# Kernel tuning notes

Measured on AMD Instinct MI355X. Metric: run time of the kernel, lower is better.

## Reference

```python
import jax, jax.numpy as jnp
import numpy as np
import math

B, S, E = 16, 4096, 16      # batch, seq_len, n_experts
NE = 64                     # config.n_embd -> expert bottleneck dim
F = 4 * NE                  # n_state = 4*n_embd -> token feature dim


def gelu(x):
    # tanh-approx GELU exactly as in the source module
    c = math.sqrt(2.0 / math.pi)
    return 0.5 * x * (1.0 + jnp.tanh(c * (x + 0.044715 * x * x * x)))


def setup_inputs() -> dict:
    key = jax.random.key(0)
    ks = jax.random.split(key, 7)
    s1 = 1.0 / math.sqrt(F)   # fan-in init like nn.Linear(F, NE)
    s2 = 1.0 / math.sqrt(NE)  # fan-in init like nn.Linear(NE, F)
    return {
        "x":  jax.random.normal(ks[0], (B, S, F), jnp.float32),
        "W1": jax.random.uniform(ks[1], (E, F, NE), jnp.float32, -s1, s1),  # stacked c_fc
        "b1": jax.random.uniform(ks[2], (E, NE),    jnp.float32, -s1, s1),
        "W2": jax.random.uniform(ks[3], (E, NE, F), jnp.float32, -s2, s2),  # stacked c_proj
        "b2": jax.random.uniform(ks[4], (E, F),     jnp.float32, -s2, s2),
        "Wg": jax.random.uniform(ks[5], (F, E),     jnp.float32, -s1, s1),  # router
        "bg": jax.random.uniform(ks[6], (E,),       jnp.float32, -s1, s1),
    }


def reference(x, W1, b1, W2, b2, Wg, bg):
    # Router: per-token scores -> mean over sequence -> softmax over experts. [B, E]
    gate = jax.nn.softmax(jnp.mean(x @ Wg + bg, axis=1), axis=-1)
    # Dense all-experts FFN: [B, E, S, NE]
    h = gelu(jnp.einsum('bsf,efh->besh', x, W1) + b1[None, :, None, :])
    # [B, E, S, F]
    outs = jnp.einsum('besh,ehf->besf', h, W2) + b2[None, :, None, :]
    # Gate-weighted combine over experts -> [B, S, F]
    return jnp.einsum('be,besf->bsf', gate, outs)
```

## Files before the change

kernel.cpp:

```cpp
#include <hip/hip_runtime.h>
#include <hip/hip_bf16.h>
#include <stdint.h>

#define NB 16
#define NS 4096
#define NF 256
#define NH 64
#define NEXP 16

typedef __attribute__((ext_vector_type(8))) short     bf16x8;
typedef __attribute__((ext_vector_type(4))) float     f32x4;
typedef __attribute__((ext_vector_type(2))) unsigned  u32x2;
typedef __attribute__((ext_vector_type(8))) unsigned short u16x8;

#define PART_OFF   0u
#define GATE_OFF   524288u
#define BIASC_OFF  525312u
#define W1T_OFF    541696u
#define W2T_OFF    1065984u

__device__ __forceinline__ unsigned short bfr(float f) {
  unsigned u = __float_as_uint(f);
  u += 0x7fffu + ((u >> 16) & 1u);
  return (unsigned short)(u >> 16);
}
__device__ __forceinline__ unsigned pk(float a, float b) {
  __hip_bfloat162 t = __float22bfloat162_rn(make_float2(a, b));
  union { __hip_bfloat162 h; unsigned u; } cv; cv.h = t; return cv.u;
}
__device__ __forceinline__ bf16x8 as_bf(f32x4 v) {
  union { f32x4 f; bf16x8 h; } u; u.f = v; return u.h;
}
__device__ __forceinline__ void stage16(const void* g, void* l) {
  __builtin_amdgcn_global_load_lds((const __attribute__((address_space(1))) void*)g,
                                   (__attribute__((address_space(3))) void*)l, 16, 0, 0);
}

__global__ void k_pre(const float* __restrict__ x, const float* __restrict__ W1,
                      const float* __restrict__ W2, uint8_t* __restrict__ wsb) {
  const int blk = blockIdx.x;
  if (blk < 512) {
    const int b  = blk >> 5;
    const int ch = blk & 31;
    const int f  = threadIdx.x;
    const float* xp = x + ((size_t)b * NS + (size_t)ch * 128) * NF + f;
    float s = 0.0f;
    for (int i = 0; i < 128; ++i) s += xp[(size_t)i * NF];
    ((float*)(wsb + PART_OFF))[(size_t)(ch * 16 + b) * NF + f] = s;
    return;
  }
  const int u = (blk - 512) * 256 + threadIdx.x;
  u16x8 vals;
  if (u < 32768) {
    const int e  = u >> 11;
    const int r  = u & 2047;
    const int hd = r >> 5;
    const int kc = r & 31;
    const float* src = W1 + (size_t)e * (NF * NH) + (size_t)(kc * 8) * NH + hd;
#pragma unroll
    for (int j = 0; j < 8; ++j) vals[j] = bfr(src[(size_t)j * NH]);
    const int dst = (kc >> 2) * 4096 + hd * 64 + (kc & 3) * 16;
    *(u16x8*)(wsb + W1T_OFF + (size_t)e * 32768 + dst) = vals;
  } else {
    const int u2 = u - 32768;
    const int e  = u2 >> 11;
    const int r  = u2 & 2047;
    const int f  = r >> 3;
    const int hc = r & 7;
    const float* src = W2 + (size_t)e * (NH * NF) + (size_t)(hc * 8) * NF + f;
#pragma unroll
    for (int j = 0; j < 8; ++j) vals[j] = bfr(src[(size_t)j * NF]);
    const int dst = hc * 4096 + f * 16;
    *(u16x8*)(wsb + W2T_OFF + (size_t)e * 32768 + dst) = vals;
  }
}

__global__ void k_gate(const float* __restrict__ Wg, const float* __restrict__ bg,
                       const float* __restrict__ b2, uint8_t* __restrict__ wsb) {
  __shared__ float cs[16][256];
  __shared__ float lg[16][16];
  __shared__ float gs[16][16];
  const float* part  = (const float*)(wsb + PART_OFF);
  float* gate  = (float*)(wsb + GATE_OFF);
  float* biasc = (float*)(wsb + BIASC_OFF);
  const int t = threadIdx.x;
  for (int b = 0; b < 16; ++b) {
    float s = 0.0f;
    for (int ch = 0; ch < 32; ++ch) s += part[(size_t)(ch * 16 + b) * NF + t];
    cs[b][t] = s * (1.0f / 4096.0f);
  }
  __syncthreads();
  {
    const int b = t >> 4, e = t & 15;
    float acc = bg[e];
    for (int f = 0; f < NF; ++f) acc += cs[b][f] * Wg[f * 16 + e];
    lg[b][e] = acc;
  }
  __syncthreads();
  {
    const int b = t >> 4, e = t & 15;
    float m = lg[b][0];
    for (int j = 1; j < 16; ++j) m = fmaxf(m, lg[b][j]);
    float den = 0.0f;
    for (int j = 0; j < 16; ++j) den += __expf(lg[b][j] - m);
    float g = __expf(lg[b][e] - m) / den;
    gate[b * 16 + e] = g;
    gs[b][e] = g;
  }
  __syncthreads();
  for (int b = 0; b < 16; ++b) {
    float acc = 0.0f;
    for (int e = 0; e < 16; ++e) acc += gs[b][e] * b2[e * NF + t];
    biasc[b * NF + t] = acc;
  }
}

__global__ __launch_bounds__(512, 2)
void k_main(const float* __restrict__ x, const float* __restrict__ b1g,
            const uint8_t* __restrict__ wsb, float* __restrict__ out) {
  __shared__ __align__(16) uint8_t lds[98304];

  const int tid  = threadIdx.x;
  const int w    = tid >> 6;
  const int lane = tid & 63;
  const int c    = lane & 15;
  const int q    = lane >> 4;
  const int r4   = w & 3;
  const bool g1  = (w < 4);
  const int blk  = blockIdx.x;
  const int b    = blk >> 5;

  const float* gate_ws = (const float*)(wsb + GATE_OFF) + b * 16;
  const float* biasc   = (const float*)(wsb + BIASC_OFF) + b * NF;
  const uint8_t* w1src = wsb + W1T_OFF;
  const uint8_t* w2src = wsb + W2T_OFF;

  const f32x4 fz = {0.0f, 0.0f, 0.0f, 0.0f};
  f32x4 R[32];

#pragma unroll
  for (int i = 0; i < 4; ++i)
    stage16(w1src + i * 8192 + tid * 16, lds + i * 8192 + tid * 16);

  if (g1) {
    const int row0 = blk * 128 + r4 * 32;
#pragma unroll
    for (int n = 0; n < 2; ++n) {
      const float* xp = x + (size_t)(row0 + n * 16 + c) * NF + q * 8;
#pragma unroll
      for (int ks = 0; ks < 8; ++ks) {
        f32x4 v0 = *(const f32x4*)(xp + ks * 32);
        f32x4 v1 = *(const f32x4*)(xp + ks * 32 + 4);
        union { unsigned u[4]; f32x4 f; } cv;
        cv.u[0] = pk(v0[0], v0[1]); cv.u[1] = pk(v0[2], v0[3]);
        cv.u[2] = pk(v1[0], v1[1]); cv.u[3] = pk(v1[2], v1[3]);
        R[8 + n * 8 + ks] = cv.f;
      }
    }
  } else {
#pragma unroll
    for (int i = 0; i < 32; ++i) R[i] = fz;
  }

  bf16x8 w2r[2][4];

  __syncthreads();

  const float K1 = -2.3021858962f;
  const float KA = -0.102942243f;

#pragma unroll 1
  for (int e = 0; e < NEXP; ++e) {
    const int p  = e & 1;
    const int pn = p ^ 1;

    if (e < 15) {
      const uint8_t* src = w1src + (size_t)(e + 1) * 32768;
      uint8_t* dst = lds + pn * 32768;
#pragma unroll
      for (int i = 0; i < 4; ++i)
        stage16(src + i * 8192 + tid * 16, dst + i * 8192 + tid * 16);
    }

    if (g1) {
      const uint8_t* w1p = lds + p * 32768;
#pragma unroll
      for (int i = 0; i < 8; ++i) R[i] = fz;
      __builtin_amdgcn_s_setprio(1);
#pragma unroll
      for (int ks = 0; ks < 8; ++ks) {
        bf16x8 am[4];
#pragma unroll
        for (int m = 0; m < 4; ++m)
          am[m] = *(const bf16x8*)(w1p + ks * 4096 + (m * 16 + c) * 64 + q * 16);
#pragma unroll
        for (int m = 0; m < 4; ++m) {
          R[m * 2 + 0] = __builtin_amdgcn_mfma_f32_16x16x32_bf16(am[m], as_bf(R[8 + ks]),     R[m * 2 + 0], 0, 0, 0);
          R[m * 2 + 1] = __builtin_amdgcn_mfma_f32_16x16x32_bf16(am[m], as_bf(R[16 + ks]),    R[m * 2 + 1], 0, 0, 0);
        }
      }
      __builtin_amdgcn_s_setprio(0);

      const float gv = gate_ws[e];
      uint8_t* htp = lds + 65536 + p * 16384;
#pragma unroll
      for (int m = 0; m < 4; ++m) {
        f32x4 b1v = *(const f32x4*)(b1g + e * NH + m * 16 + q * 4);
#pragma unroll
        for (int n = 0; n < 2; ++n) {
          f32x4 hv = R[m * 2 + n] + b1v;
          float o[4];
#pragma unroll
          for (int r = 0; r < 4; ++r) {
            float xx = hv[r];
            float x2 = xx * xx;
            float tt = fmaf(KA, x2, K1);
            float ez = __builtin_amdgcn_exp2f(xx * tt);
            float rc = __builtin_amdgcn_rcpf(ez + 1.0f);
            o[r] = (gv * xx) * rc;
          }
          u32x2 hw;
          hw.x = pk(o[0], o[1]);
          hw.y = pk(o[2], o[3]);
          const int chunk = m * 2 + (q >> 1);
          const int tok   = r4 * 32 + n * 16 + c;
          *(u32x2*)(htp + chunk * 2048 + tok * 16 + (q & 1) * 8) = hw;
        }
      }
    } else {
      if (e > 0) {
        const uint8_t* htp2 = lds + 65536 + pn * 16384;
        __builtin_amdgcn_s_setprio(1);
#pragma unroll
        for (int ks2 = 0; ks2 < 2; ++ks2) {
          bf16x8 bb2[8];
#pragma unroll
          for (int n2 = 0; n2 < 8; ++n2)
            bb2[n2] = *(const bf16x8*)(htp2 + (ks2 * 4 + q) * 2048 + (n2 * 16 + c) * 16);
#pragma unroll
          for (int m2 = 0; m2 < 4; ++m2)
#pragma unroll
            for (int n2 = 0; n2 < 8; ++n2)
              R[m2 * 8 + n2] = __builtin_amdgcn_mfma_f32_16x16x32_bf16(w2r[ks2][m2], bb2[n2], R[m2 * 8 + n2], 0, 0, 0);
        }
        __builtin_amdgcn_s_setprio(0);
      }
      const uint8_t* src = w2src + (size_t)e * 32768 + q * 4096 + (r4 * 64 + c) * 16;
#pragma unroll
      for (int ks2 = 0; ks2 < 2; ++ks2)
#pragma unroll
        for (int m2 = 0; m2 < 4; ++m2)
          w2r[ks2][m2] = *(const bf16x8*)(src + ks2 * 16384 + m2 * 256);
    }

    __syncthreads();
  }

  if (!g1) {
    const uint8_t* htp2 = lds + 65536 + 16384;
#pragma unroll
    for (int ks2 = 0; ks2 < 2; ++ks2) {
      bf16x8 bb2[8];
#pragma unroll
      for (int n2 = 0; n2 < 8; ++n2)
        bb2[n2] = *(const bf16x8*)(htp2 + (ks2 * 4 + q) * 2048 + (n2 * 16 + c) * 16);
#pragma unroll
      for (int m2 = 0; m2 < 4; ++m2)
#pragma unroll
        for (int n2 = 0; n2 < 8; ++n2)
          R[m2 * 8 + n2] = __builtin_amdgcn_mfma_f32_16x16x32_bf16(w2r[ks2][m2], bb2[n2], R[m2 * 8 + n2], 0, 0, 0);
    }
#pragma unroll
    for (int m2 = 0; m2 < 4; ++m2) {
      const int fbase = r4 * 64 + m2 * 16 + q * 4;
      f32x4 bc = *(const f32x4*)(biasc + fbase);
#pragma unroll
      for (int n2 = 0; n2 < 8; ++n2) {
        const int token = blk * 128 + n2 * 16 + c;
        f32x4 o = R[m2 * 8 + n2] + bc;
        *(f32x4*)(out + (size_t)token * NF + fbase) = o;
      }
    }
  }
}

extern "C" void kernel_launch(void* const* d_in, const int* in_sizes, int n_in,
                              void* d_out, int out_size, void* d_ws, size_t ws_size,
                              hipStream_t stream) {
  const float* x  = (const float*)d_in[0];
  const float* W1 = (const float*)d_in[1];
  const float* b1 = (const float*)d_in[2];
  const float* W2 = (const float*)d_in[3];
  const float* b2 = (const float*)d_in[4];
  const float* Wg = (const float*)d_in[5];
  const float* bg = (const float*)d_in[6];
  float* out = (float*)d_out;
  uint8_t* wsb = (uint8_t*)d_ws;

  k_pre<<<768, 256, 0, stream>>>(x, W1, W2, wsb);
  k_gate<<<1, 256, 0, stream>>>(Wg, bg, b2, wsb);
  k_main<<<512, 512, 0, stream>>>(x, b1, wsb, out);
}
```

Measured before the change: 126.7 us.

## Skew GELU epilogue one expert behind GEMM1 with triple-buffered hidden tiles

Restructures the expert loop so the first warp group runs expert e's GEMM1 while writing the GELU epilogue for expert e-1. The hidden buffer grows from double to triple (more LDS), and the second warp group consumes hidden tiles two experts behind. The loop is unrolled by two so register slots are fixed at compile time, and W2 fragments are held in the shared R array. The goal is to overlap transcendental epilogue work with MFMA work and lengthen the pipeline, at the cost of more LDS, which may limit occupancy at two blocks per CU, and more register pressure.

Result: slower. 130.4 us (+3.0%).

```diff
diff --git a/kernel.cpp b/kernel.cpp
--- a/kernel.cpp
+++ b/kernel.cpp
@@ -115,18 +115,105 @@
   }
 }
 
+
+template<int PAR>
+__device__ __forceinline__ void g1_gemm(int e, f32x4 (&R)[40], float (&gvv)[2],
+                                        const uint8_t* ldsb, const float* b1g,
+                                        const float* gate_ws, int c, int q) {
+#pragma unroll
+  for (int m = 0; m < 4; ++m)
+    R[32 + PAR * 4 + m] = *(const f32x4*)(b1g + e * NH + m * 16 + q * 4);
+  gvv[PAR] = gate_ws[e];
+  const uint8_t* w1p = ldsb + PAR * 32768;
+  const f32x4 fz = {0.0f, 0.0f, 0.0f, 0.0f};
+#pragma unroll
+  for (int i = 0; i < 8; ++i) R[16 + PAR * 8 + i] = fz;
+  __builtin_amdgcn_s_setprio(1);
+#pragma unroll
+  for (int ks = 0; ks < 8; ++ks) {
+    bf16x8 am[4];
+#pragma unroll
+    for (int m = 0; m < 4; ++m)
+      am[m] = *(const bf16x8*)(w1p + ks * 4096 + (m * 16 + c) * 64 + q * 16);
+#pragma unroll
+    for (int m = 0; m < 4; ++m) {
+      R[16 + PAR * 8 + m * 2 + 0] = __builtin_amdgcn_mfma_f32_16x16x32_bf16(am[m], as_bf(R[ks]),     R[16 + PAR * 8 + m * 2 + 0], 0, 0, 0);
+      R[16 + PAR * 8 + m * 2 + 1] = __builtin_amdgcn_mfma_f32_16x16x32_bf16(am[m], as_bf(R[8 + ks]), R[16 + PAR * 8 + m * 2 + 1], 0, 0, 0);
+    }
+  }
+  __builtin_amdgcn_s_setprio(0);
+}
+
+template<int PPREV>
+__device__ __forceinline__ void g1_epilogue(int eprev, f32x4 (&R)[40], const float (&gvv)[2],
+                                            uint8_t* ldsb, int w, int c, int q) {
+  const float K1 = -2.3021858962f;
+  const float KA = -0.102942243f;
+  const float gv = gvv[PPREV];
+  uint8_t* htp = ldsb + 65536 + (eprev % 3) * 16384;
+#pragma unroll
+  for (int m = 0; m < 4; ++m) {
+    f32x4 b1v = R[32 + PPREV * 4 + m];
+#pragma unroll
+    for (int n = 0; n < 2; ++n) {
+      f32x4 hv = R[16 + PPREV * 8 + m * 2 + n] + b1v;
+      float o[4];
+#pragma unroll
+      for (int r = 0; r < 4; ++r) {
+        float xx = hv[r];
+        float tt = fmaf(KA, xx * xx, K1);
+        float ez = __builtin_amdgcn_exp2f(xx * tt);
+        o[r] = (gv * xx) * __builtin_amdgcn_rcpf(ez + 1.0f);
+      }
+      u32x2 hw;
+      hw.x = pk(o[0], o[1]);
+      hw.y = pk(o[2], o[3]);
+      const int chunk = m * 2 + (q >> 1);
+      const int tok   = w * 32 + n * 16 + c;
+      *(u32x2*)(htp + chunk * 2048 + tok * 16 + (q & 1) * 8) = hw;
+    }
+  }
+}
+
+__device__ __forceinline__ void g2_gemm2(f32x4 (&R)[40], const uint8_t* htp2, int c, int q) {
+#pragma unroll
+  for (int ks2 = 0; ks2 < 2; ++ks2) {
+    bf16x8 bb[8];
+#pragma unroll
+    for (int n2 = 0; n2 < 8; ++n2)
+      bb[n2] = *(const bf16x8*)(htp2 + (ks2 * 4 + q) * 2048 + (n2 * 16 + c) * 16);
+    __builtin_amdgcn_s_setprio(1);
+#pragma unroll
+    for (int m2 = 0; m2 < 4; ++m2)
+#pragma unroll
+      for (int n2 = 0; n2 < 8; ++n2)
+        R[m2 * 8 + n2] = __builtin_amdgcn_mfma_f32_16x16x32_bf16(as_bf(R[32 + ks2 * 4 + m2]), bb[n2], R[m2 * 8 + n2], 0, 0, 0);
+    __builtin_amdgcn_s_setprio(0);
+  }
+}
+
+__device__ __forceinline__ void g2_loadw2(f32x4 (&R)[40], const uint8_t* w2src, int e,
+                                          int fs, int c, int q) {
+  const uint8_t* src = w2src + (size_t)e * 32768 + q * 4096 + (fs + c) * 16;
+#pragma unroll
+  for (int ks2 = 0; ks2 < 2; ++ks2)
+#pragma unroll
+    for (int m2 = 0; m2 < 4; ++m2)
+      R[32 + ks2 * 4 + m2] = *(const f32x4*)(src + ks2 * 16384 + m2 * 256);
+}
+
 __global__ __launch_bounds__(512, 2)
 void k_main(const float* __restrict__ x, const float* __restrict__ b1g,
             const uint8_t* __restrict__ wsb, float* __restrict__ out) {
-  __shared__ __align__(16) uint8_t lds[98304];
+  __shared__ __align__(16) uint8_t lds[114688];
 
   const int tid  = threadIdx.x;
   const int w    = tid >> 6;
   const int lane = tid & 63;
   const int c    = lane & 15;
   const int q    = lane >> 4;
-  const int r4   = w & 3;
   const bool g1  = (w < 4);
+  const int fs   = (w - 4) * 64;
   const int blk  = blockIdx.x;
   const int b    = blk >> 5;
 
@@ -135,15 +222,15 @@
   const uint8_t* w1src = wsb + W1T_OFF;
   const uint8_t* w2src = wsb + W2T_OFF;
 
-  const f32x4 fz = {0.0f, 0.0f, 0.0f, 0.0f};
-  f32x4 R[32];
+  f32x4 R[40];
+  float gvv[2];
 
 #pragma unroll
   for (int i = 0; i < 4; ++i)
     stage16(w1src + i * 8192 + tid * 16, lds + i * 8192 + tid * 16);
 
   if (g1) {
-    const int row0 = blk * 128 + r4 * 32;
+    const int row0 = blk * 128 + w * 32;
 #pragma unroll
     for (int n = 0; n < 2; ++n) {
       const float* xp = x + (size_t)(row0 + n * 16 + c) * NF + q * 8;
@@ -154,125 +241,69 @@
         union { unsigned u[4]; f32x4 f; } cv;
         cv.u[0] = pk(v0[0], v0[1]); cv.u[1] = pk(v0[2], v0[3]);
         cv.u[2] = pk(v1[0], v1[1]); cv.u[3] = pk(v1[2], v1[3]);
-        R[8 + n * 8 + ks] = cv.f;
+        R[n * 8 + ks] = cv.f;
       }
     }
   } else {
+    const f32x4 fz = {0.0f, 0.0f, 0.0f, 0.0f};
 #pragma unroll
     for (int i = 0; i < 32; ++i) R[i] = fz;
   }
 
-  bf16x8 w2r[2][4];
-
-  __syncthreads();
-
-  const float K1 = -2.3021858962f;
-  const float KA = -0.102942243f;
+  __syncthreads();
 
 #pragma unroll 1
-  for (int e = 0; e < NEXP; ++e) {
-    const int p  = e & 1;
-    const int pn = p ^ 1;
-
-    if (e < 15) {
-      const uint8_t* src = w1src + (size_t)(e + 1) * 32768;
-      uint8_t* dst = lds + pn * 32768;
-#pragma unroll
-      for (int i = 0; i < 4; ++i)
-        stage16(src + i * 8192 + tid * 16, dst + i * 8192 + tid * 16);
-    }
-
-    if (g1) {
-      const uint8_t* w1p = lds + p * 32768;
-#pragma unroll
-      for (int i = 0; i < 8; ++i) R[i] = fz;
-      __builtin_amdgcn_s_setprio(1);
-#pragma unroll
-      for (int ks = 0; ks < 8; ++ks) {
-        bf16x8 am[4];
-#pragma unroll
-        for (int m = 0; m < 4; ++m)
-          am[m] = *(const bf16x8*)(w1p + ks * 4096 + (m * 16 + c) * 64 + q * 16);
-#pragma unroll
-        for (int m = 0; m < 4; ++m) {
-          R[m * 2 + 0] = __builtin_amdgcn_mfma_f32_16x16x32_bf16(am[m], as_bf(R[8 + ks]),     R[m * 2 + 0], 0, 0, 0);
-          R[m * 2 + 1] = __builtin_amdgcn_mfma_f32_16x16x32_bf16(am[m], as_bf(R[16 + ks]),    R[m * 2 + 1], 0, 0, 0);
-        }
-      }
-      __builtin_amdgcn_s_setprio(0);
-
-      const float gv = gate_ws[e];
-      uint8_t* htp = lds + 65536 + p * 16384;
-#pragma unroll
-      for (int m = 0; m < 4; ++m) {
-        f32x4 b1v = *(const f32x4*)(b1g + e * NH + m * 16 + q * 4);
-#pragma unroll
-        for (int n = 0; n < 2; ++n) {
-          f32x4 hv = R[m * 2 + n] + b1v;
-          float o[4];
-#pragma unroll
-          for (int r = 0; r < 4; ++r) {
-            float xx = hv[r];
-            float x2 = xx * xx;
-            float tt = fmaf(KA, x2, K1);
-            float ez = __builtin_amdgcn_exp2f(xx * tt);
-            float rc = __builtin_amdgcn_rcpf(ez + 1.0f);
-            o[r] = (gv * xx) * rc;
-          }
-          u32x2 hw;
-          hw.x = pk(o[0], o[1]);
-          hw.y = pk(o[2], o[3]);
-          const int chunk = m * 2 + (q >> 1);
-          const int tok   = r4 * 32 + n * 16 + c;
-          *(u32x2*)(htp + chunk * 2048 + tok * 16 + (q & 1) * 8) = hw;
-        }
-      }
-    } else {
-      if (e > 0) {
-        const uint8_t* htp2 = lds + 65536 + pn * 16384;
-        __builtin_amdgcn_s_setprio(1);
-#pragma unroll
-        for (int ks2 = 0; ks2 < 2; ++ks2) {
-          bf16x8 bb2[8];
-#pragma unroll
-          for (int n2 = 0; n2 < 8; ++n2)
-            bb2[n2] = *(const bf16x8*)(htp2 + (ks2 * 4 + q) * 2048 + (n2 * 16 + c) * 16);
-#pragma unroll
-          for (int m2 = 0; m2 < 4; ++m2)
-#pragma unroll
-            for (int n2 = 0; n2 < 8; ++n2)
-              R[m2 * 8 + n2] = __builtin_amdgcn_mfma_f32_16x16x32_bf16(w2r[ks2][m2], bb2[n2], R[m2 * 8 + n2], 0, 0, 0);
-        }
-        __builtin_amdgcn_s_setprio(0);
-      }
-      const uint8_t* src = w2src + (size_t)e * 32768 + q * 4096 + (r4 * 64 + c) * 16;
-#pragma unroll
-      for (int ks2 = 0; ks2 < 2; ++ks2)
-#pragma unroll
-        for (int m2 = 0; m2 < 4; ++m2)
-          w2r[ks2][m2] = *(const bf16x8*)(src + ks2 * 16384 + m2 * 256);
-    }
-
-    __syncthreads();
-  }
-
+  for (int eb = 0; eb < 8; ++eb) {
+    {
+      const int e = 2 * eb;
+      if (e < 15) {
+        const uint8_t* src = w1src + (size_t)(e + 1) * 32768;
+        uint8_t* dst = lds + 32768;
+#pragma unroll
+        for (int i = 0; i < 4; ++i)
+          stage16(src + i * 8192 + tid * 16, dst + i * 8192 + tid * 16);
+      }
+      if (g1) {
+        g1_gemm<0>(e, R, gvv, lds, b1g, gate_ws, c, q);
+        if (e > 0) g1_epilogue<1>(e - 1, R, gvv, lds, w, c, q);
+      } else {
+        if (e >= 2) g2_gemm2(R, lds + 65536 + ((e - 2) % 3) * 16384, c, q);
+        if (e >= 1) g2_loadw2(R, w2src, e - 1, fs, c, q);
+      }
+      __syncthreads();
+    }
+    {
+      const int e = 2 * eb + 1;
+      if (e < 15) {
+        const uint8_t* src = w1src + (size_t)(e + 1) * 32768;
+        uint8_t* dst = lds;
+#pragma unroll
+        for (int i = 0; i < 4; ++i)
+          stage16(src + i * 8192 + tid * 16, dst + i * 8192 + tid * 16);
+      }
+      if (g1) {
+        g1_gemm<1>(e, R, gvv, lds, b1g, gate_ws, c, q);
+        g1_epilogue<0>(e - 1, R, gvv, lds, w, c, q);
+      } else {
+        if (e >= 2) g2_gemm2(R, lds + 65536 + ((e - 2) % 3) * 16384, c, q);
+        g2_loadw2(R, w2src, e - 1, fs, c, q);
+      }
+      __syncthreads();
+    }
+  }
+
+  if (g1) {
+    g1_epilogue<1>(15, R, gvv, lds, w, c, q);
+  } else {
+    g2_gemm2(R, lds + 65536 + 2 * 16384, c, q);
+    g2_loadw2(R, w2src, 15, fs, c, q);
+  }
+  __syncthreads();
   if (!g1) {
-    const uint8_t* htp2 = lds + 65536 + 16384;
-#pragma unroll
-    for (int ks2 = 0; ks2 < 2; ++ks2) {
-      bf16x8 bb2[8];
-#pragma unroll
-      for (int n2 = 0; n2 < 8; ++n2)
-        bb2[n2] = *(const bf16x8*)(htp2 + (ks2 * 4 + q) * 2048 + (n2 * 16 + c) * 16);
-#pragma unroll
-      for (int m2 = 0; m2 < 4; ++m2)
-#pragma unroll
-        for (int n2 = 0; n2 < 8; ++n2)
-          R[m2 * 8 + n2] = __builtin_amdgcn_mfma_f32_16x16x32_bf16(w2r[ks2][m2], bb2[n2], R[m2 * 8 + n2], 0, 0, 0);
-    }
+    g2_gemm2(R, lds + 65536, c, q);
 #pragma unroll
     for (int m2 = 0; m2 < 4; ++m2) {
-      const int fbase = r4 * 64 + m2 * 16 + q * 4;
+      const int fbase = fs + m2 * 16 + q * 4;
       f32x4 bc = *(const f32x4*)(biasc + fbase);
 #pragma unroll
       for (int n2 = 0; n2 < 8; ++n2) {
```
